# Performance work log

Hardware: AMD Instinct MI355X
Metric: run time of the kernel (lower is better)

Reference implementation:

```python
import jax, jax.numpy as jnp
import numpy as np

BETA = 0.25
N_E = 4096
E_DIM = 64
B, T = 16, 1024


def setup_inputs() -> dict:
    key = jax.random.key(0)
    k1, k2 = jax.random.split(key)
    z = jax.random.normal(k1, (B, T, E_DIM), dtype=jnp.float32)
    # embedding.weight.data.uniform_(-1/n_e, 1/n_e)
    codebook = jax.random.uniform(k2, (N_E, E_DIM), dtype=jnp.float32,
                                  minval=-1.0 / N_E, maxval=1.0 / N_E)
    return {"z": z, "codebook": codebook}


def reference(z, codebook):
    # z: (B, T, e_dim), codebook: (n_e, e_dim)
    n_e, e_dim = codebook.shape
    zf = z.reshape(-1, e_dim)  # (N, e_dim)

    # d[n, k] = ||z_n||^2 + ||e_k||^2 - 2 z_n . e_k   -> (N, n_e)
    d = (jnp.sum(zf * zf, axis=1, keepdims=True)
         + jnp.sum(codebook * codebook, axis=1)
         - 2.0 * jnp.matmul(zf, codebook.T))

    idx = jnp.argmin(d, axis=1)                  # (N,) int
    z_q = codebook[idx].reshape(z.shape)         # (B, T, e_dim)

    sg = jax.lax.stop_gradient
    loss = jnp.mean((z_q - sg(z)) ** 2) + BETA * jnp.mean((sg(z_q) - z) ** 2)

    # straight-through estimator
    z_q_st = z + sg(z_q - z)

    # e_mean = mean over tokens of one-hot encodings == normalized code counts
    n_tokens = idx.shape[0]
    counts = jnp.zeros((n_e,), dtype=z.dtype).at[idx].add(1.0)
    e_mean = counts / n_tokens
    perplexity = jnp.exp(-jnp.sum(e_mean * jnp.log(e_mean + 1e-10)))

    return (loss, z_q_st, idx, perplexity)
```

## Files before the change

### kernel.cpp

```cpp
#include <hip/hip_runtime.h>
#include <math.h>

#define N_TOK   16384
#define EDIM    64
#define NE      4096
#define NSLICE  16
#define TPB     256
#define ZQ_OFF  1
#define IDX_OFF (1 + N_TOK * EDIM)
#define PERP_OFF (IDX_OFF + N_TOK)

typedef unsigned long long u64;

__global__ __launch_bounds__(256) void norms_zero_kernel(
    const float* __restrict__ z, const float* __restrict__ cb,
    float* __restrict__ nz, float* __restrict__ ne,
    int* __restrict__ hist, float* __restrict__ lossAcc) {
#pragma clang fp contract(off)
    int i = blockIdx.x * 256 + threadIdx.x;
    if (i < NE) hist[i] = 0;
    if (i == 0) lossAcc[0] = 0.0f;
    const float* row;
    float* dst;
    if (i < N_TOK)            { row = z  + (size_t)i * EDIM;           dst = nz + i; }
    else if (i < N_TOK + NE)  { row = cb + (size_t)(i - N_TOK) * EDIM; dst = ne + (i - N_TOK); }
    else return;

    float r[8];
#pragma unroll
    for (int j = 0; j < 8; ++j) { float v = row[j]; r[j] = v * v; }
#pragma unroll
    for (int b = 8; b < 64; b += 8) {
#pragma unroll
        for (int j = 0; j < 8; ++j) { float v = row[b + j]; r[j] = r[j] + v * v; }
    }
    dst[0] = ((r[0] + r[1]) + (r[2] + r[3])) + ((r[4] + r[5]) + (r[6] + r[7]));
}

__global__ __launch_bounds__(256, 2) void dist_argmin_kernel(
    const float* __restrict__ z, const float* __restrict__ cb,
    const float* __restrict__ nz, const float* __restrict__ ne,
    u64* __restrict__ part) {
    __shared__ float4 zt[2048];
    __shared__ float4 ct[2048];
    const int tid   = threadIdx.x;
    const int tg    = tid & 15;
    const int cg    = tid >> 4;
    const int bx    = blockIdx.x;
    const int slice = blockIdx.y;
    const int tok0  = bx * 128;

    {
        const float4* zp = (const float4*)z + (size_t)tok0 * 16;
#pragma unroll
        for (int r = 0; r < 8; ++r) {
            const int f   = tid * 8 + r;
            const int tl  = f >> 4;
            const int q   = f & 15;
            const int row = q * 8 + (tl & 7);
            const int col = (tl >> 3) ^ (row & 15);
            zt[row * 16 + col] = zp[f];
        }
    }

    float tnz[8];
#pragma unroll
    for (int i = 0; i < 8; ++i) tnz[i] = nz[tok0 + tg * 8 + i];

    u64 best[8];
#pragma unroll
    for (int i = 0; i < 8; ++i) best[i] = ~0ull;

#pragma unroll 1
    for (int c = 0; c < 2; ++c) {
        const int kbase = slice * 256 + c * 128;
        {
            const float4* cp = (const float4*)cb + (size_t)kbase * 16;
#pragma unroll
            for (int r = 0; r < 8; ++r) {
                const int f   = tid * 8 + r;
                const int lc  = f >> 4;
                const int q   = f & 15;
                const int row = q * 8 + (lc & 7);
                const int col = (lc >> 3) ^ (row & 15);
                ct[row * 16 + col] = cp[f];
            }
        }
        float sne[8];
#pragma unroll
        for (int j = 0; j < 8; ++j) sne[j] = ne[kbase + cg * 8 + j];
        __syncthreads();

        float acc[8][8];
#pragma unroll
        for (int i = 0; i < 8; ++i)
#pragma unroll
            for (int j = 0; j < 8; ++j) acc[i][j] = 0.0f;

#pragma unroll
        for (int q = 0; q < 16; ++q) {
            float4 zf[8], cf[8];
#pragma unroll
            for (int i = 0; i < 8; ++i) {
                const int row = q * 8 + i;
                zf[i] = zt[row * 16 + (tg ^ (row & 15))];
            }
#pragma unroll
            for (int j = 0; j < 8; ++j) {
                const int row = q * 8 + j;
                cf[j] = ct[row * 16 + (cg ^ (row & 15))];
            }
#pragma unroll
            for (int i = 0; i < 8; ++i)
#pragma unroll
                for (int j = 0; j < 8; ++j) {
                    acc[i][j] = __builtin_fmaf(zf[i].x, cf[j].x, acc[i][j]);
                    acc[i][j] = __builtin_fmaf(zf[i].y, cf[j].y, acc[i][j]);
                    acc[i][j] = __builtin_fmaf(zf[i].z, cf[j].z, acc[i][j]);
                    acc[i][j] = __builtin_fmaf(zf[i].w, cf[j].w, acc[i][j]);
                }
        }

#pragma unroll
        for (int i = 0; i < 8; ++i)
#pragma unroll
            for (int j = 0; j < 8; ++j) {
                const float d = __builtin_fmaf(-2.0f, acc[i][j], tnz[i] + sne[j]);
                const u64 p = ((u64)__float_as_uint(d) << 32)
                            | (u64)(kbase + cg * 8 + j);
                if (p < best[i]) best[i] = p;
            }
        __syncthreads();
    }

    u64* red = (u64*)ct;
#pragma unroll
    for (int i = 0; i < 8; ++i) red[cg * 128 + tg * 8 + i] = best[i];
    __syncthreads();
    if (tid < 128) {
        u64 b = red[tid];
#pragma unroll
        for (int s = 1; s < 16; ++s) {
            const u64 p = red[s * 128 + tid];
            if (p < b) b = p;
        }
        part[(size_t)slice * N_TOK + tok0 + tid] = b;
    }
}

__global__ __launch_bounds__(256) void reduce_gather_kernel(
    const float* __restrict__ z, const float* __restrict__ cb,
    const u64* __restrict__ part, int* __restrict__ hist,
    float* __restrict__ lossAcc, float* __restrict__ out) {
    const int t = blockIdx.x * 256 + threadIdx.x;
    u64 best = part[t];
#pragma unroll
    for (int s = 1; s < NSLICE; ++s) {
        u64 p = part[(size_t)s * N_TOK + t];
        if (p < best) best = p;
    }
    const int idx = (int)(best & 0xFFFFFFFFull);
    out[IDX_OFF + t] = (float)idx;
    atomicAdd(&hist[idx], 1);

    const float4* ev = (const float4*)(cb + (size_t)idx * EDIM);
    const float4* zv = (const float4*)(z + (size_t)t * EDIM);
    float* o = out + ZQ_OFF + (size_t)t * EDIM;
    float acc = 0.0f;
#pragma unroll
    for (int j = 0; j < 16; ++j) {
        float4 e = ev[j], zz = zv[j];
        float d;
        d = e.x - zz.x; o[4 * j + 0] = zz.x + d; acc = __builtin_fmaf(d, d, acc);
        d = e.y - zz.y; o[4 * j + 1] = zz.y + d; acc = __builtin_fmaf(d, d, acc);
        d = e.z - zz.z; o[4 * j + 2] = zz.z + d; acc = __builtin_fmaf(d, d, acc);
        d = e.w - zz.w; o[4 * j + 3] = zz.w + d; acc = __builtin_fmaf(d, d, acc);
    }
    __shared__ float red[256];
    red[threadIdx.x] = acc;
    __syncthreads();
    for (int s = 128; s > 0; s >>= 1) {
        if (threadIdx.x < s) red[threadIdx.x] += red[threadIdx.x + s];
        __syncthreads();
    }
    if (threadIdx.x == 0) atomicAdd(lossAcc, red[0]);
}

__global__ __launch_bounds__(256) void finalize_kernel(
    const int* __restrict__ hist, const float* __restrict__ lossAcc,
    float* __restrict__ out) {
    __shared__ float red[256];
    float acc = 0.0f;
    for (int i = threadIdx.x; i < NE; i += 256) {
        float e = (float)hist[i] * (1.0f / 16384.0f);
        acc += e * logf(e + 1e-10f);
    }
    red[threadIdx.x] = acc;
    __syncthreads();
    for (int s = 128; s > 0; s >>= 1) {
        if (threadIdx.x < s) red[threadIdx.x] += red[threadIdx.x + s];
        __syncthreads();
    }
    if (threadIdx.x == 0) {
        out[PERP_OFF] = expf(-red[0]);
        float m = lossAcc[0] * (1.0f / 1048576.0f);
        out[0] = m + 0.25f * m;
    }
}

extern "C" void kernel_launch(void* const* d_in, const int* in_sizes, int n_in,
                              void* d_out, int out_size, void* d_ws, size_t ws_size,
                              hipStream_t stream) {
    const float* z  = (const float*)d_in[0];
    const float* cb = (const float*)d_in[1];
    float* out = (float*)d_out;

    char* ws = (char*)d_ws;
    u64*   part    = (u64*)ws;
    float* nz      = (float*)(ws + (size_t)NSLICE * N_TOK * 8);
    float* ne      = nz + N_TOK;
    int*   hist    = (int*)(ne + NE);
    float* lossAcc = (float*)(hist + NE);

    hipLaunchKernelGGL(norms_zero_kernel, dim3(80), dim3(256), 0, stream,
                       z, cb, nz, ne, hist, lossAcc);
    hipLaunchKernelGGL(dist_argmin_kernel,
                       dim3(N_TOK / 128, NSLICE), dim3(TPB), 0, stream,
                       z, cb, nz, ne, part);
    hipLaunchKernelGGL(reduce_gather_kernel, dim3(64), dim3(256), 0, stream,
                       z, cb, part, hist, lossAcc, out);
    hipLaunchKernelGGL(finalize_kernel, dim3(1), dim3(256), 0, stream,
                       hist, lossAcc, out);
}
```

Before: 195.5 us.

## Enlarge distance tile to 256x256 with 16x16 per-thread register blocking

Each thread block now covers 256 tokens by 256 codes, and each thread holds a 16x16 accumulator tile instead of 8x8 for two chunks. Both tiles are loaded once into a new XOR-swizzled shared layout, which removes the inner chunk loop and its barriers. The argmin becomes a float compare with a final pack, instead of a 64-bit compare for every element. This raises FMA-to-LDS-load intensity, but 256 accumulators per thread push register use near the limit with launch bounds of 1, cutting occupancy and risking spills. The grid also halves to 1024 blocks.

After: 295.0 us. 50.9% more time.

```diff
diff --git a/kernel.cpp b/kernel.cpp
--- a/kernel.cpp
+++ b/kernel.cpp
@@ -37,115 +37,93 @@
     dst[0] = ((r[0] + r[1]) + (r[2] + r[3])) + ((r[4] + r[5]) + (r[6] + r[7]));
 }
 
-__global__ __launch_bounds__(256, 2) void dist_argmin_kernel(
+__global__ __launch_bounds__(256, 1) void dist_argmin_kernel(
     const float* __restrict__ z, const float* __restrict__ cb,
     const float* __restrict__ nz, const float* __restrict__ ne,
     u64* __restrict__ part) {
-    __shared__ float4 zt[2048];
-    __shared__ float4 ct[2048];
+    __shared__ float4 zt[4096];
+    __shared__ float4 ct[4096];
     const int tid   = threadIdx.x;
     const int tg    = tid & 15;
     const int cg    = tid >> 4;
-    const int bx    = blockIdx.x;
-    const int slice = blockIdx.y;
-    const int tok0  = bx * 128;
+    const int tok0  = blockIdx.x * 256;
+    const int kbase = blockIdx.y * 256;
 
     {
-        const float4* zp = (const float4*)z + (size_t)tok0 * 16;
-#pragma unroll
-        for (int r = 0; r < 8; ++r) {
-            const int f   = tid * 8 + r;
-            const int tl  = f >> 4;
+        const float4* zp = (const float4*)z  + (size_t)tok0  * 16;
+        const float4* cp = (const float4*)cb + (size_t)kbase * 16;
+#pragma unroll
+        for (int r = 0; r < 16; ++r) {
+            const int f   = r * 256 + tid;
+            const int row = f >> 4;
             const int q   = f & 15;
-            const int row = q * 8 + (tl & 7);
-            const int col = (tl >> 3) ^ (row & 15);
-            zt[row * 16 + col] = zp[f];
+            zt[q * 256 + (row ^ q)] = zp[f];
+            ct[q * 256 + (row ^ q)] = cp[f];
         }
     }
-
-    float tnz[8];
-#pragma unroll
-    for (int i = 0; i < 8; ++i) tnz[i] = nz[tok0 + tg * 8 + i];
-
-    u64 best[8];
-#pragma unroll
-    for (int i = 0; i < 8; ++i) best[i] = ~0ull;
+    __syncthreads();
+
+    float acc[16][16];
+#pragma unroll
+    for (int i = 0; i < 16; ++i)
+#pragma unroll
+        for (int j = 0; j < 16; ++j) acc[i][j] = 0.0f;
 
 #pragma unroll 1
-    for (int c = 0; c < 2; ++c) {
-        const int kbase = slice * 256 + c * 128;
-        {
-            const float4* cp = (const float4*)cb + (size_t)kbase * 16;
-#pragma unroll
-            for (int r = 0; r < 8; ++r) {
-                const int f   = tid * 8 + r;
-                const int lc  = f >> 4;
-                const int q   = f & 15;
-                const int row = q * 8 + (lc & 7);
-                const int col = (lc >> 3) ^ (row & 15);
-                ct[row * 16 + col] = cp[f];
+    for (int q = 0; q < 16; ++q) {
+        const float4* zq = zt + q * 256;
+        const float4* cq = ct + q * 256;
+        const int tgq = tg ^ q;
+        const int cgq = cg ^ q;
+        float4 cf[16];
+#pragma unroll
+        for (int j = 0; j < 16; ++j) cf[j] = cq[16 * j + cgq];
+#pragma unroll
+        for (int i = 0; i < 16; ++i) {
+            const float4 zf = zq[16 * i + tgq];
+#pragma unroll
+            for (int j = 0; j < 16; ++j) {
+                acc[i][j] = __builtin_fmaf(zf.x, cf[j].x, acc[i][j]);
+                acc[i][j] = __builtin_fmaf(zf.y, cf[j].y, acc[i][j]);
+                acc[i][j] = __builtin_fmaf(zf.z, cf[j].z, acc[i][j]);
+                acc[i][j] = __builtin_fmaf(zf.w, cf[j].w, acc[i][j]);
             }
         }
-        float sne[8];
-#pragma unroll
-        for (int j = 0; j < 8; ++j) sne[j] = ne[kbase + cg * 8 + j];
-        __syncthreads();
-
-        float acc[8][8];
-#pragma unroll
-        for (int i = 0; i < 8; ++i)
-#pragma unroll
-            for (int j = 0; j < 8; ++j) acc[i][j] = 0.0f;
-
-#pragma unroll
-        for (int q = 0; q < 16; ++q) {
-            float4 zf[8], cf[8];
-#pragma unroll
-            for (int i = 0; i < 8; ++i) {
-                const int row = q * 8 + i;
-                zf[i] = zt[row * 16 + (tg ^ (row & 15))];
-            }
-#pragma unroll
-            for (int j = 0; j < 8; ++j) {
-                const int row = q * 8 + j;
-                cf[j] = ct[row * 16 + (cg ^ (row & 15))];
-            }
-#pragma unroll
-            for (int i = 0; i < 8; ++i)
-#pragma unroll
-                for (int j = 0; j < 8; ++j) {
-                    acc[i][j] = __builtin_fmaf(zf[i].x, cf[j].x, acc[i][j]);
-                    acc[i][j] = __builtin_fmaf(zf[i].y, cf[j].y, acc[i][j]);
-                    acc[i][j] = __builtin_fmaf(zf[i].z, cf[j].z, acc[i][j]);
-                    acc[i][j] = __builtin_fmaf(zf[i].w, cf[j].w, acc[i][j]);
-                }
+    }
+
+    float tnz[16];
+#pragma unroll
+    for (int i = 0; i < 16; ++i) tnz[i] = nz[tok0 + 16 * i + tg];
+    float sne[16];
+#pragma unroll
+    for (int j = 0; j < 16; ++j) sne[j] = ne[kbase + 16 * j + cg];
+
+    u64 pb[16];
+#pragma unroll
+    for (int i = 0; i < 16; ++i) {
+        float bd = __builtin_fmaf(-2.0f, acc[i][0], tnz[i] + sne[0]);
+        int   bk = kbase + cg;
+#pragma unroll
+        for (int j = 1; j < 16; ++j) {
+            const float d = __builtin_fmaf(-2.0f, acc[i][j], tnz[i] + sne[j]);
+            const int   k = kbase + 16 * j + cg;
+            if (d < bd) { bd = d; bk = k; }
         }
-
-#pragma unroll
-        for (int i = 0; i < 8; ++i)
-#pragma unroll
-            for (int j = 0; j < 8; ++j) {
-                const float d = __builtin_fmaf(-2.0f, acc[i][j], tnz[i] + sne[j]);
-                const u64 p = ((u64)__float_as_uint(d) << 32)
-                            | (u64)(kbase + cg * 8 + j);
-                if (p < best[i]) best[i] = p;
-            }
-        __syncthreads();
-    }
-
+        pb[i] = ((u64)__float_as_uint(bd) << 32) | (u64)bk;
+    }
+
+    __syncthreads();
     u64* red = (u64*)ct;
 #pragma unroll
-    for (int i = 0; i < 8; ++i) red[cg * 128 + tg * 8 + i] = best[i];
-    __syncthreads();
-    if (tid < 128) {
-        u64 b = red[tid];
-#pragma unroll
-        for (int s = 1; s < 16; ++s) {
-            const u64 p = red[s * 128 + tid];
-            if (p < b) b = p;
-        }
-        part[(size_t)slice * N_TOK + tok0 + tid] = b;
-    }
+    for (int i = 0; i < 16; ++i) red[cg * 256 + 16 * i + tg] = pb[i];
+    __syncthreads();
+    u64 b = red[tid];
+#pragma unroll
+    for (int s = 1; s < 16; ++s) {
+        const u64 p = red[s * 256 + tid];
+        if (p < b) b = p;
+    }
+    part[(size_t)blockIdx.y * N_TOK + tok0 + tid] = b;
 }
 
 __global__ __launch_bounds__(256) void reduce_gather_kernel(
@@ -225,7 +203,7 @@
     hipLaunchKernelGGL(norms_zero_kernel, dim3(80), dim3(256), 0, stream,
                        z, cb, nz, ne, hist, lossAcc);
     hipLaunchKernelGGL(dist_argmin_kernel,
-                       dim3(N_TOK / 128, NSLICE), dim3(TPB), 0, stream,
+                       dim3(N_TOK / 256, NSLICE), dim3(TPB), 0, stream,
                        z, cb, nz, ne, part);
     hipLaunchKernelGGL(reduce_gather_kernel, dim3(64), dim3(256), 0, stream,
                        z, cb, part, hist, lossAcc, out);
```
